# Kernel optimization log

Measured on AMD Instinct MI355X. Metric: run time of the kernel, lower is better.

## Reference

```python
import jax, jax.numpy as jnp
import numpy as np

V, E = 50000, 800000
NODE_IN, EDGE_IN, OUT, HEADS = 128, 16, 32, 4
NEG_SLOPE = 0.2  # DGL EdgeGATConv default negative_slope


def setup_inputs() -> dict:
    key = jax.random.key(0)
    ks = jax.random.split(key, 10)
    return {
        "node_feats": jax.random.normal(ks[0], (V, NODE_IN), jnp.float32),
        "edge_feats": jax.random.normal(ks[1], (E, EDGE_IN), jnp.float32),
        "src": jax.random.randint(ks[2], (E,), 0, V),
        "dst": jax.random.randint(ks[3], (E,), 0, V),
        "W_node": jax.random.normal(ks[4], (NODE_IN, HEADS * OUT), jnp.float32) * 0.05,
        "W_edge": jax.random.normal(ks[5], (EDGE_IN, HEADS * OUT), jnp.float32) * 0.05,
        "attn_l": jax.random.normal(ks[6], (HEADS, OUT), jnp.float32) * 0.05,
        "attn_r": jax.random.normal(ks[7], (HEADS, OUT), jnp.float32) * 0.05,
        "attn_e": jax.random.normal(ks[8], (HEADS, OUT), jnp.float32) * 0.05,
        "res_W": jax.random.normal(ks[9], (NODE_IN, HEADS * OUT), jnp.float32) * 0.05,
        "bias": jnp.zeros((HEADS * OUT,), jnp.float32),
    }


def _leaky_relu(x, slope):
    return jnp.where(x >= 0, x, slope * x)


def reference(node_feats, edge_feats, src, dst, W_node, W_edge, attn_l, attn_r, attn_e, res_W, bias):
    V = node_feats.shape[0]
    H, F = attn_l.shape
    # linear projections
    ft = (node_feats @ W_node).reshape(V, H, F)    # [V,H,F]
    fe = (edge_feats @ W_edge).reshape(-1, H, F)   # [E,H,F]
    # per-head attention logits
    el = jnp.einsum('vhf,hf->vh', ft, attn_l)      # [V,H]
    er = jnp.einsum('vhf,hf->vh', ft, attn_r)      # [V,H]
    ee = jnp.einsum('ehf,hf->eh', fe, attn_e)      # [E,H]
    e = _leaky_relu(el[src] + er[dst] + ee, NEG_SLOPE)  # [E,H]
    # edge softmax over incoming edges of each destination node (stable)
    emax = jax.ops.segment_max(e, dst, num_segments=V)  # [V,H]
    ex = jnp.exp(e - emax[dst])
    esum = jax.ops.segment_sum(ex, dst, num_segments=V)  # [V,H]
    a = ex / esum[dst]                                   # [E,H]
    # weighted message passing: u_mul_e(ft, a) then sum to dst
    msg = ft[src] * a[:, :, None]                        # [E,H,F]
    rst = jax.ops.segment_sum(msg, dst, num_segments=V)  # [V,H,F]
    # residual connection + bias (EdgeGATConv residual=True, bias=True)
    rst = rst + (node_feats @ res_W).reshape(V, H, F)
    rst = rst + bias.reshape(1, H, F)
    # agg_mode='flatten': concat heads
    return rst.reshape(V, H * F)
```

## Files before the change

### kernel.cpp

```cpp
#include <hip/hip_runtime.h>
#include <hip/hip_fp16.h>
#include <cstdint>

#define V_N 50000
#define E_N 800000
#define NODE_IN 128
#define EDGE_IN 16
#define HF 128
#define NEG_SLOPE 0.2f
#define NB_SCAN 196

#define OFF_FT    0
#define OFF_EL    3200000
#define OFF_ER    3400000
#define OFF_DEG   3600000
#define OFF_ROW   3650000
#define OFF_BSUM  3700004
#define OFF_RANK  3700260
#define OFF_REC   4500260
#define OFF_WATT  7700260
#define OFF_BFRAG 7700324

typedef short bf16x8 __attribute__((ext_vector_type(8)));
typedef float f32x4 __attribute__((ext_vector_type(4)));

__device__ __forceinline__ unsigned short f2bf(float f) {
    unsigned u = __float_as_uint(f);
    u += 0x7fffu + ((u >> 16) & 1u);
    return (unsigned short)(u >> 16);
}
__device__ __forceinline__ unsigned pk2(float lo, float hi) {
    return (unsigned)f2bf(lo) | ((unsigned)f2bf(hi) << 16);
}
__device__ __forceinline__ float bflo(unsigned w) { return __uint_as_float(w << 16); }
__device__ __forceinline__ float bfhi(unsigned w) { return __uint_as_float(w & 0xffff0000u); }

typedef __fp16 fp16x2 __attribute__((ext_vector_type(2)));
__device__ __forceinline__ unsigned pkh2(float a, float b) {
    fp16x2 h = __builtin_amdgcn_cvt_pkrtz(a, b);
    return __builtin_bit_cast(unsigned, h);
}
__device__ __forceinline__ __half2 u2h(unsigned u) {
    return __builtin_bit_cast(__half2, u);
}
__device__ __forceinline__ unsigned h2u(__half2 h) {
    return __builtin_bit_cast(unsigned, h);
}

__global__ void k_prep(const float* __restrict__ We,
                       const float* __restrict__ attn_e,
                       const float* __restrict__ Wn,
                       const float* __restrict__ Wr,
                       float* __restrict__ watt,
                       unsigned* __restrict__ bfrag,
                       int* __restrict__ deg) {
    int g = blockIdx.x * 256 + threadIdx.x;
    for (int i = g; i < V_N; i += 16384) deg[i] = 0;
    if (blockIdx.x == 0 && threadIdx.x < 64) {
        int k = threadIdx.x >> 2, h = threadIdx.x & 3;
        float s = 0.f;
        #pragma unroll
        for (int f = 0; f < 32; f++)
            s += We[k * HF + h * 32 + f] * attn_e[h * 32 + f];
        watt[k * 4 + h] = s;
    }
    if (g < 16384) {
        int c    = g >> 8;
        int lane = (g >> 2) & 63;
        int jp   = g & 3;
        int nt = c >> 2, ks = c & 3;
        int col = nt * 16 + (lane & 15);
        int k   = ks * 32 + (lane >> 4) * 8 + jp * 2;
        const float* W = (col < 128) ? Wn : Wr;
        int cc = col & 127;
        float x0 = W[(size_t)k * 128 + cc];
        float x1 = W[(size_t)(k + 1) * 128 + cc];
        bfrag[g] = pk2(x0, x1);
    }
}

__global__ __launch_bounds__(256) void k_node(
    const float* __restrict__ nf, const unsigned* __restrict__ bfragw,
    const float* __restrict__ attn_l, const float* __restrict__ attn_r,
    const float* __restrict__ bias,
    unsigned* __restrict__ ftw, float* __restrict__ el,
    float* __restrict__ er, float* __restrict__ out)
{
    __shared__ __align__(16) float sSf[32 * 140];
    unsigned short* sA = (unsigned short*)sSf;

    const int t = threadIdx.x;
    const int lane = t & 63;
    const int w = t >> 6;
    const int nb = blockIdx.x * 32;
    const int n15 = lane & 15;
    const int q = lane >> 4;
    const unsigned short* bfrag = (const unsigned short*)bfragw;

    #pragma unroll
    for (int i = 0; i < 4; i++) {
        int f = t + i * 256;
        int node = f >> 5;
        int kc = (f & 31) * 4;
        float4 v = {0.f, 0.f, 0.f, 0.f};
        if (nb + node < V_N)
            v = *(const float4*)(nf + (size_t)(nb + node) * NODE_IN + kc);
        uint2 u2 = make_uint2(pk2(v.x, v.y), pk2(v.z, v.w));
        *(uint2*)&sA[node * 136 + kc] = u2;
    }
    __syncthreads();

    f32x4 acc[2][4];
    #pragma unroll
    for (int m = 0; m < 2; m++)
        #pragma unroll
        for (int tt = 0; tt < 4; tt++) acc[m][tt] = (f32x4){0.f, 0.f, 0.f, 0.f};

    #pragma unroll
    for (int ks = 0; ks < 4; ks++) {
        bf16x8 a0 = *(const bf16x8*)&sA[n15 * 136 + ks * 32 + q * 8];
        bf16x8 a1 = *(const bf16x8*)&sA[(16 + n15) * 136 + ks * 32 + q * 8];
        #pragma unroll
        for (int tt = 0; tt < 4; tt++) {
            int nt = (tt < 2) ? (2 * w + tt) : (8 + 2 * w + (tt - 2));
            bf16x8 b = *(const bf16x8*)(bfrag + ((size_t)(nt * 4 + ks) * 64 + lane) * 8);
            acc[0][tt] = __builtin_amdgcn_mfma_f32_16x16x32_bf16(a0, b, acc[0][tt], 0, 0, 0);
            acc[1][tt] = __builtin_amdgcn_mfma_f32_16x16x32_bf16(a1, b, acc[1][tt], 0, 0, 0);
        }
    }

    {
        float al0 = attn_l[w * 32 + n15];
        float al1 = attn_l[w * 32 + 16 + n15];
        float ar0 = attn_r[w * 32 + n15];
        float ar1 = attn_r[w * 32 + 16 + n15];
        #pragma unroll
        for (int m = 0; m < 2; m++) {
            #pragma unroll
            for (int r = 0; r < 4; r++) {
                float fa = acc[m][0][r], fb = acc[m][1][r];
                float elp = fa * al0 + fb * al1;
                float erp = fa * ar0 + fb * ar1;
                elp += __shfl_xor(elp, 1); erp += __shfl_xor(erp, 1);
                elp += __shfl_xor(elp, 2); erp += __shfl_xor(erp, 2);
                elp += __shfl_xor(elp, 4); erp += __shfl_xor(erp, 4);
                elp += __shfl_xor(elp, 8); erp += __shfl_xor(erp, 8);
                int node = nb + m * 16 + q * 4 + r;
                if (n15 == 0 && node < V_N) {
                    el[node * 4 + w] = elp;
                    er[node * 4 + w] = erp;
                }
            }
        }
    }
    #pragma unroll
    for (int m = 0; m < 2; m++)
        #pragma unroll
        for (int r = 0; r < 4; r++) {
            int node = nb + m * 16 + q * 4 + r;
            if (node < V_N)
                ftw[(size_t)node * 64 + w * 16 + n15] =
                    pkh2(acc[m][0][r], acc[m][1][r]);
        }
    __syncthreads();

    #pragma unroll
    for (int m = 0; m < 2; m++)
        #pragma unroll
        for (int tt = 2; tt < 4; tt++)
            #pragma unroll
            for (int r = 0; r < 4; r++)
                sSf[(m * 16 + q * 4 + r) * 140 + w * 32 + (tt - 2) * 16 + n15] =
                    acc[m][tt][r];
    __syncthreads();
    #pragma unroll
    for (int i = 0; i < 4; i++) {
        int u = t + i * 256;
        int node = u >> 5, c4 = (u & 31) * 4;
        if (nb + node < V_N) {
            float4 v = *(float4*)&sSf[node * 140 + c4];
            float4 b4 = *(const float4*)(bias + c4);
            v.x += b4.x; v.y += b4.y; v.z += b4.z; v.w += b4.w;
            *(float4*)(out + (size_t)(nb + node) * HF + c4) = v;
        }
    }
}

__global__ void k_hist(const int* __restrict__ dst, int* __restrict__ deg,
                       int* __restrict__ rank) {
    int e = blockIdx.x * 256 + threadIdx.x;
    if (e < E_N) rank[e] = atomicAdd(&deg[dst[e]], 1);
}

__global__ __launch_bounds__(256) void k_scan1(const int* __restrict__ deg,
                                               int* __restrict__ rowp,
                                               int* __restrict__ bsum) {
    __shared__ int sh[256];
    int t = threadIdx.x, b = blockIdx.x;
    int i = b * 256 + t;
    int v = (i < V_N) ? deg[i] : 0;
    sh[t] = v;
    __syncthreads();
    #pragma unroll
    for (int off = 1; off < 256; off <<= 1) {
        int u = (t >= off) ? sh[t - off] : 0;
        __syncthreads();
        sh[t] += u;
        __syncthreads();
    }
    if (i < V_N) rowp[i] = sh[t] - v;
    if (t == 255) bsum[b] = sh[255];
}

__global__ __launch_bounds__(256) void k_scan23(int* __restrict__ rowp,
                                                const int* __restrict__ bsum) {
    __shared__ int sh[256];
    int t = threadIdx.x, b = blockIdx.x;
    int v = (t < NB_SCAN) ? bsum[t] : 0;
    sh[t] = v;
    __syncthreads();
    #pragma unroll
    for (int off = 1; off < 256; off <<= 1) {
        int u = (t >= off) ? sh[t - off] : 0;
        __syncthreads();
        sh[t] += u;
        __syncthreads();
    }
    int boff = (b == 0) ? 0 : sh[b - 1];
    int i = b * 256 + t;
    if (i < V_N) rowp[i] += boff;
    if (i == 0) rowp[V_N] = E_N;
}

__global__ __launch_bounds__(256) void k_escatter(
    const float* __restrict__ ef, const int* __restrict__ src,
    const int* __restrict__ dst, const int* __restrict__ rank,
    const int* __restrict__ rowp, const float* __restrict__ watt,
    const float* __restrict__ el, uint4* __restrict__ rec)
{
    __shared__ float sw[64];
    __shared__ __align__(16) float see[256][4];
    const int t = threadIdx.x;
    if (t < 64) sw[t] = watt[t];
    __syncthreads();
    const int base = blockIdx.x * 256;
    const int lane = t & 63, w = t >> 6;
    const int k0 = (lane & 3) * 4;

    #pragma unroll
    for (int r = 0; r < 4; r++) {
        int le = w * 64 + r * 16 + (lane >> 2);
        float4 v = *(const float4*)(ef + (size_t)(base + le) * EDGE_IN + k0);
        float e0 = 0.f, e1 = 0.f, e2 = 0.f, e3 = 0.f;
        float vv[4] = {v.x, v.y, v.z, v.w};
        #pragma unroll
        for (int j = 0; j < 4; j++) {
            int k = k0 + j;
            e0 += vv[j] * sw[k * 4 + 0];
            e1 += vv[j] * sw[k * 4 + 1];
            e2 += vv[j] * sw[k * 4 + 2];
            e3 += vv[j] * sw[k * 4 + 3];
        }
        e0 += __shfl_xor(e0, 1); e1 += __shfl_xor(e1, 1);
        e2 += __shfl_xor(e2, 1); e3 += __shfl_xor(e3, 1);
        e0 += __shfl_xor(e0, 2); e1 += __shfl_xor(e1, 2);
        e2 += __shfl_xor(e2, 2); e3 += __shfl_xor(e3, 2);
        if ((lane & 3) == 0) {
            float4 o = {e0, e1, e2, e3};
            *(float4*)&see[le][0] = o;
        }
    }
    __syncthreads();

    int e = base + t;
    int s = src[e], d = dst[e];
    int p = rowp[d] + rank[e];
    float4 ee = *(float4*)&see[t][0];
    float4 el4 = *(const float4*)(el + (size_t)s * 4);
    uint4 rr;
    rr.x = (unsigned)s;
    rr.y = pk2(el4.x + ee.x, el4.y + ee.y);
    rr.z = pk2(el4.z + ee.z, el4.w + ee.w);
    rr.w = 0;
    rec[p] = rr;
}

__global__ __launch_bounds__(256) void k_gather(
    const int* __restrict__ row, const uint4* __restrict__ rec,
    const float* __restrict__ er,
    const unsigned* __restrict__ ftw, float* __restrict__ out)
{
    __shared__ unsigned aw[4][64][4];
    const int lane = threadIdx.x & 63;
    const int wid  = threadIdx.x >> 6;
    const int d = blockIdx.x * 4 + wid;
    if (d >= V_N) return;
    const int n0 = row[d];
    const int deg = row[d + 1] - n0;
    if (deg == 0) return;

    const float4 er4 = *(const float4*)(er + (size_t)d * 4);

    const int qw = lane >> 4, li = lane & 15;
    const int head = li >> 2;
    float4 s4 = {0.f, 0.f, 0.f, 0.f};
    __half2 ha0 = u2h(0u), ha1 = u2h(0u), ha2 = u2h(0u), ha3 = u2h(0u);
    __half2 hb0 = u2h(0u), hb1 = u2h(0u), hb2 = u2h(0u), hb3 = u2h(0u);

    for (int i0 = 0; i0 < deg; i0 += 64) {
        int chunk = min(64, deg - i0);
        int si = 0;
        float4 ex = {0.f, 0.f, 0.f, 0.f};
        if (lane < chunk) {
            uint4 r = rec[n0 + i0 + lane];
            si = (int)r.x;
            float x0 = bflo(r.y) + er4.x;
            float x1 = bfhi(r.y) + er4.y;
            float x2 = bflo(r.z) + er4.z;
            float x3 = bfhi(r.z) + er4.w;
            x0 = x0 >= 0.f ? x0 : NEG_SLOPE * x0;
            x1 = x1 >= 0.f ? x1 : NEG_SLOPE * x1;
            x2 = x2 >= 0.f ? x2 : NEG_SLOPE * x2;
            x3 = x3 >= 0.f ? x3 : NEG_SLOPE * x3;
            ex.x = __expf(x0); ex.y = __expf(x1);
            ex.z = __expf(x2); ex.w = __expf(x3);
            s4.x += ex.x; s4.y += ex.y; s4.z += ex.z; s4.w += ex.w;
        }
        uint4 ap;
        ap.x = pkh2(ex.x, ex.x); ap.y = pkh2(ex.y, ex.y);
        ap.z = pkh2(ex.z, ex.z); ap.w = pkh2(ex.w, ex.w);
        *(uint4*)&aw[wid][lane][0] = ap;
        asm volatile("s_waitcnt lgkmcnt(0)" ::: "memory");

        int iters = (chunk + 7) & ~7;
        for (int j = 0; j < iters; j += 8) {
            int jq0 = j + qw, jq1 = j + qw + 4;
            int sidx0 = __shfl(si, jq0);
            int sidx1 = __shfl(si, jq1);
            unsigned au0 = aw[wid][jq0][head];
            unsigned au1 = aw[wid][jq1][head];
            uint4 wv0 = *(const uint4*)(ftw + (size_t)sidx0 * 64 + li * 4);
            uint4 wv1 = *(const uint4*)(ftw + (size_t)sidx1 * 64 + li * 4);
            ha0 = __hfma2(u2h(wv0.x), u2h(au0), ha0);
            ha1 = __hfma2(u2h(wv0.y), u2h(au0), ha1);
            ha2 = __hfma2(u2h(wv0.z), u2h(au0), ha2);
            ha3 = __hfma2(u2h(wv0.w), u2h(au0), ha3);
            hb0 = __hfma2(u2h(wv1.x), u2h(au1), hb0);
            hb1 = __hfma2(u2h(wv1.y), u2h(au1), hb1);
            hb2 = __hfma2(u2h(wv1.z), u2h(au1), hb2);
            hb3 = __hfma2(u2h(wv1.w), u2h(au1), hb3);
        }
    }
    #pragma unroll
    for (int off = 1; off < 64; off <<= 1) {
        s4.x += __shfl_xor(s4.x, off);
        s4.y += __shfl_xor(s4.y, off);
        s4.z += __shfl_xor(s4.z, off);
        s4.w += __shfl_xor(s4.w, off);
    }
    ha0 = __hadd2(ha0, hb0); ha1 = __hadd2(ha1, hb1);
    ha2 = __hadd2(ha2, hb2); ha3 = __hadd2(ha3, hb3);
    ha0 = __hadd2(ha0, u2h(__shfl_xor(h2u(ha0), 16)));
    ha1 = __hadd2(ha1, u2h(__shfl_xor(h2u(ha1), 16)));
    ha2 = __hadd2(ha2, u2h(__shfl_xor(h2u(ha2), 16)));
    ha3 = __hadd2(ha3, u2h(__shfl_xor(h2u(ha3), 16)));
    ha0 = __hadd2(ha0, u2h(__shfl_xor(h2u(ha0), 32)));
    ha1 = __hadd2(ha1, u2h(__shfl_xor(h2u(ha1), 32)));
    ha2 = __hadd2(ha2, u2h(__shfl_xor(h2u(ha2), 32)));
    ha3 = __hadd2(ha3, u2h(__shfl_xor(h2u(ha3), 32)));
    if (qw == 0) {
        float rsv = 1.f / (head == 0 ? s4.x : head == 1 ? s4.y :
                           head == 2 ? s4.z : s4.w);
        float* op = out + (size_t)d * HF + head * 32 + (li & 3) * 4;
        float4 r0 = *(float4*)op;
        r0.x += __low2float(ha0) * rsv; r0.y += __low2float(ha1) * rsv;
        r0.z += __low2float(ha2) * rsv; r0.w += __low2float(ha3) * rsv;
        *(float4*)op = r0;
        float4 r1 = *(float4*)(op + 16);
        r1.x += __high2float(ha0) * rsv; r1.y += __high2float(ha1) * rsv;
        r1.z += __high2float(ha2) * rsv; r1.w += __high2float(ha3) * rsv;
        *(float4*)(op + 16) = r1;
    }
}

extern "C" void kernel_launch(void* const* d_in, const int* in_sizes, int n_in,
                              void* d_out, int out_size, void* d_ws, size_t ws_size,
                              hipStream_t stream) {
    const float* nf     = (const float*)d_in[0];
    const float* ef     = (const float*)d_in[1];
    const int*   src    = (const int*)d_in[2];
    const int*   dst    = (const int*)d_in[3];
    const float* Wn     = (const float*)d_in[4];
    const float* We     = (const float*)d_in[5];
    const float* attn_l = (const float*)d_in[6];
    const float* attn_r = (const float*)d_in[7];
    const float* attn_e = (const float*)d_in[8];
    const float* Wr     = (const float*)d_in[9];
    const float* bias   = (const float*)d_in[10];
    float* out = (float*)d_out;

    unsigned* wsw  = (unsigned*)d_ws;
    unsigned* ftw  = wsw + OFF_FT;
    float* el      = (float*)(wsw + OFF_EL);
    float* er      = (float*)(wsw + OFF_ER);
    int* deg       = (int*)(wsw + OFF_DEG);
    int* rowp      = (int*)(wsw + OFF_ROW);
    int* bsum      = (int*)(wsw + OFF_BSUM);
    int* rank      = (int*)(wsw + OFF_RANK);
    uint4* rec     = (uint4*)(wsw + OFF_REC);
    float* watt    = (float*)(wsw + OFF_WATT);
    unsigned* bfrag = wsw + OFF_BFRAG;

    k_prep<<<64, 256, 0, stream>>>(We, attn_e, Wn, Wr, watt, bfrag, deg);
    k_hist<<<(E_N + 255) / 256, 256, 0, stream>>>(dst, deg, rank);
    k_scan1<<<NB_SCAN, 256, 0, stream>>>(deg, rowp, bsum);
    k_scan23<<<NB_SCAN, 256, 0, stream>>>(rowp, bsum);
    k_node<<<(V_N + 31) / 32, 256, 0, stream>>>(nf, bfrag, attn_l, attn_r,
                                                bias, ftw, el, er, out);
    k_escatter<<<E_N / 256, 256, 0, stream>>>(ef, src, dst, rank,
                                              rowp, watt, el, rec);
    k_gather<<<(V_N + 3) / 4, 256, 0, stream>>>(rowp, rec, er, ftw, out);
}
```

Before: 245.1 us.

## Fuse histogram, scan and edge scatter into one cooperative persistent kernel

New measurement: 609.3 us. 149% more time.

```diff
diff --git a/kernel.cpp b/kernel.cpp
--- a/kernel.cpp
+++ b/kernel.cpp
@@ -1,6 +1,9 @@
 #include <hip/hip_runtime.h>
 #include <hip/hip_fp16.h>
+#include <hip/hip_cooperative_groups.h>
 #include <cstdint>
+
+namespace cg = cooperative_groups;
 
 #define V_N 50000
 #define E_N 800000
@@ -16,9 +19,7 @@
 #define OFF_DEG   3600000
 #define OFF_ROW   3650000
 #define OFF_BSUM  3700004
-#define OFF_RANK  3700260
 #define OFF_REC   4500260
-#define OFF_WATT  7700260
 #define OFF_BFRAG 7700324
 
 typedef short bf16x8 __attribute__((ext_vector_type(8)));
@@ -47,23 +48,10 @@
     return __builtin_bit_cast(unsigned, h);
 }
 
-__global__ void k_prep(const float* __restrict__ We,
-                       const float* __restrict__ attn_e,
-                       const float* __restrict__ Wn,
+__global__ void k_prep(const float* __restrict__ Wn,
                        const float* __restrict__ Wr,
-                       float* __restrict__ watt,
-                       unsigned* __restrict__ bfrag,
-                       int* __restrict__ deg) {
+                       unsigned* __restrict__ bfrag) {
     int g = blockIdx.x * 256 + threadIdx.x;
-    for (int i = g; i < V_N; i += 16384) deg[i] = 0;
-    if (blockIdx.x == 0 && threadIdx.x < 64) {
-        int k = threadIdx.x >> 2, h = threadIdx.x & 3;
-        float s = 0.f;
-        #pragma unroll
-        for (int f = 0; f < 32; f++)
-            s += We[k * HF + h * 32 + f] * attn_e[h * 32 + f];
-        watt[k * 4 + h] = s;
-    }
     if (g < 16384) {
         int c    = g >> 8;
         int lane = (g >> 2) & 63;
@@ -186,103 +174,124 @@
     }
 }
 
-__global__ void k_hist(const int* __restrict__ dst, int* __restrict__ deg,
-                       int* __restrict__ rank) {
-    int e = blockIdx.x * 256 + threadIdx.x;
-    if (e < E_N) rank[e] = atomicAdd(&deg[dst[e]], 1);
-}
-
-__global__ __launch_bounds__(256) void k_scan1(const int* __restrict__ deg,
-                                               int* __restrict__ rowp,
-                                               int* __restrict__ bsum) {
-    __shared__ int sh[256];
-    int t = threadIdx.x, b = blockIdx.x;
-    int i = b * 256 + t;
-    int v = (i < V_N) ? deg[i] : 0;
-    sh[t] = v;
-    __syncthreads();
-    #pragma unroll
-    for (int off = 1; off < 256; off <<= 1) {
-        int u = (t >= off) ? sh[t - off] : 0;
-        __syncthreads();
-        sh[t] += u;
-        __syncthreads();
-    }
-    if (i < V_N) rowp[i] = sh[t] - v;
-    if (t == 255) bsum[b] = sh[255];
-}
-
-__global__ __launch_bounds__(256) void k_scan23(int* __restrict__ rowp,
-                                                const int* __restrict__ bsum) {
-    __shared__ int sh[256];
-    int t = threadIdx.x, b = blockIdx.x;
-    int v = (t < NB_SCAN) ? bsum[t] : 0;
-    sh[t] = v;
-    __syncthreads();
-    #pragma unroll
-    for (int off = 1; off < 256; off <<= 1) {
-        int u = (t >= off) ? sh[t - off] : 0;
-        __syncthreads();
-        sh[t] += u;
-        __syncthreads();
-    }
-    int boff = (b == 0) ? 0 : sh[b - 1];
-    int i = b * 256 + t;
-    if (i < V_N) rowp[i] += boff;
-    if (i == 0) rowp[V_N] = E_N;
-}
-
-__global__ __launch_bounds__(256) void k_escatter(
+__global__ __launch_bounds__(256, 4) void k_build(
     const float* __restrict__ ef, const int* __restrict__ src,
-    const int* __restrict__ dst, const int* __restrict__ rank,
-    const int* __restrict__ rowp, const float* __restrict__ watt,
-    const float* __restrict__ el, uint4* __restrict__ rec)
+    const int* __restrict__ dst, const float* __restrict__ We,
+    const float* __restrict__ attn_e, const float* __restrict__ el,
+    int* __restrict__ deg, int* __restrict__ rowp,
+    int* __restrict__ bsum, uint4* __restrict__ rec)
 {
+    cg::grid_group grid = cg::this_grid();
     __shared__ float sw[64];
     __shared__ __align__(16) float see[256][4];
+    __shared__ int shs[256];
     const int t = threadIdx.x;
-    if (t < 64) sw[t] = watt[t];
-    __syncthreads();
-    const int base = blockIdx.x * 256;
+    const int b = blockIdx.x;
+    const int G = gridDim.x;
+
+    if (t < 64) {
+        int k = t >> 2, h = t & 3;
+        float s = 0.f;
+        #pragma unroll
+        for (int f = 0; f < 32; f++)
+            s += We[k * HF + h * 32 + f] * attn_e[h * 32 + f];
+        sw[t] = s;
+    }
+    for (int i = b * 256 + t; i < V_N; i += G * 256) deg[i] = 0;
+    grid.sync();
+
     const int lane = t & 63, w = t >> 6;
     const int k0 = (lane & 3) * 4;
-
-    #pragma unroll
-    for (int r = 0; r < 4; r++) {
-        int le = w * 64 + r * 16 + (lane >> 2);
-        float4 v = *(const float4*)(ef + (size_t)(base + le) * EDGE_IN + k0);
-        float e0 = 0.f, e1 = 0.f, e2 = 0.f, e3 = 0.f;
-        float vv[4] = {v.x, v.y, v.z, v.w};
-        #pragma unroll
-        for (int j = 0; j < 4; j++) {
-            int k = k0 + j;
-            e0 += vv[j] * sw[k * 4 + 0];
-            e1 += vv[j] * sw[k * 4 + 1];
-            e2 += vv[j] * sw[k * 4 + 2];
-            e3 += vv[j] * sw[k * 4 + 3];
-        }
-        e0 += __shfl_xor(e0, 1); e1 += __shfl_xor(e1, 1);
-        e2 += __shfl_xor(e2, 1); e3 += __shfl_xor(e3, 1);
-        e0 += __shfl_xor(e0, 2); e1 += __shfl_xor(e1, 2);
-        e2 += __shfl_xor(e2, 2); e3 += __shfl_xor(e3, 2);
-        if ((lane & 3) == 0) {
-            float4 o = {e0, e1, e2, e3};
-            *(float4*)&see[le][0] = o;
-        }
-    }
-    __syncthreads();
-
-    int e = base + t;
-    int s = src[e], d = dst[e];
-    int p = rowp[d] + rank[e];
-    float4 ee = *(float4*)&see[t][0];
-    float4 el4 = *(const float4*)(el + (size_t)s * 4);
-    uint4 rr;
-    rr.x = (unsigned)s;
-    rr.y = pk2(el4.x + ee.x, el4.y + ee.y);
-    rr.z = pk2(el4.z + ee.z, el4.w + ee.w);
-    rr.w = 0;
-    rec[p] = rr;
+    int sv[4], dv[4], rv[4];
+    unsigned lA[4], lB[4];
+    int ntile = 0;
+
+    for (int tile = b; tile < E_N / 256; tile += G) {
+        const int base = tile * 256;
+        #pragma unroll
+        for (int r = 0; r < 4; r++) {
+            int le = w * 64 + r * 16 + (lane >> 2);
+            float4 v = *(const float4*)(ef + (size_t)(base + le) * EDGE_IN + k0);
+            float e0 = 0.f, e1 = 0.f, e2 = 0.f, e3 = 0.f;
+            float vv[4] = {v.x, v.y, v.z, v.w};
+            #pragma unroll
+            for (int j = 0; j < 4; j++) {
+                int k = k0 + j;
+                e0 += vv[j] * sw[k * 4 + 0];
+                e1 += vv[j] * sw[k * 4 + 1];
+                e2 += vv[j] * sw[k * 4 + 2];
+                e3 += vv[j] * sw[k * 4 + 3];
+            }
+            e0 += __shfl_xor(e0, 1); e1 += __shfl_xor(e1, 1);
+            e2 += __shfl_xor(e2, 1); e3 += __shfl_xor(e3, 1);
+            e0 += __shfl_xor(e0, 2); e1 += __shfl_xor(e1, 2);
+            e2 += __shfl_xor(e2, 2); e3 += __shfl_xor(e3, 2);
+            if ((lane & 3) == 0) {
+                float4 o = {e0, e1, e2, e3};
+                *(float4*)&see[le][0] = o;
+            }
+        }
+        __syncthreads();
+        int e = base + t;
+        int s = src[e], d = dst[e];
+        float4 ee = *(float4*)&see[t][0];
+        float4 el4 = *(const float4*)(el + (size_t)s * 4);
+        sv[ntile] = s;
+        dv[ntile] = d;
+        rv[ntile] = atomicAdd(&deg[d], 1);
+        lA[ntile] = pk2(el4.x + ee.x, el4.y + ee.y);
+        lB[ntile] = pk2(el4.z + ee.z, el4.w + ee.w);
+        ntile++;
+        __syncthreads();
+    }
+    grid.sync();
+
+    if (b < NB_SCAN) {
+        int i = b * 256 + t;
+        int v = (i < V_N) ? deg[i] : 0;
+        shs[t] = v;
+        __syncthreads();
+        #pragma unroll
+        for (int off = 1; off < 256; off <<= 1) {
+            int u = (t >= off) ? shs[t - off] : 0;
+            __syncthreads();
+            shs[t] += u;
+            __syncthreads();
+        }
+        if (i < V_N) rowp[i] = shs[t] - v;
+        if (t == 255) bsum[b] = shs[255];
+    }
+    grid.sync();
+    if (b < NB_SCAN) {
+        int v = (t < NB_SCAN) ? bsum[t] : 0;
+        shs[t] = v;
+        __syncthreads();
+        #pragma unroll
+        for (int off = 1; off < 256; off <<= 1) {
+            int u = (t >= off) ? shs[t - off] : 0;
+            __syncthreads();
+            shs[t] += u;
+            __syncthreads();
+        }
+        int boff = (b == 0) ? 0 : shs[b - 1];
+        int i = b * 256 + t;
+        if (i < V_N) rowp[i] += boff;
+        if (i == 0) rowp[V_N] = E_N;
+    }
+    grid.sync();
+
+    #pragma unroll
+    for (int u = 0; u < 4; u++) {
+        if (u < ntile) {
+            int p = rowp[dv[u]] + rv[u];
+            uint4 rr;
+            rr.x = (unsigned)sv[u];
+            rr.y = lA[u];
+            rr.z = lB[u];
+            rr.w = 0;
+            rec[p] = rr;
+        }
+    }
 }
 
 __global__ __launch_bounds__(256) void k_gather(
@@ -406,18 +415,18 @@
     int* deg       = (int*)(wsw + OFF_DEG);
     int* rowp      = (int*)(wsw + OFF_ROW);
     int* bsum      = (int*)(wsw + OFF_BSUM);
-    int* rank      = (int*)(wsw + OFF_RANK);
     uint4* rec     = (uint4*)(wsw + OFF_REC);
-    float* watt    = (float*)(wsw + OFF_WATT);
     unsigned* bfrag = wsw + OFF_BFRAG;
 
-    k_prep<<<64, 256, 0, stream>>>(We, attn_e, Wn, Wr, watt, bfrag, deg);
-    k_hist<<<(E_N + 255) / 256, 256, 0, stream>>>(dst, deg, rank);
-    k_scan1<<<NB_SCAN, 256, 0, stream>>>(deg, rowp, bsum);
-    k_scan23<<<NB_SCAN, 256, 0, stream>>>(rowp, bsum);
+    k_prep<<<64, 256, 0, stream>>>(Wn, Wr, bfrag);
     k_node<<<(V_N + 31) / 32, 256, 0, stream>>>(nf, bfrag, attn_l, attn_r,
                                                 bias, ftw, el, er, out);
-    k_escatter<<<E_N / 256, 256, 0, stream>>>(ef, src, dst, rank,
-                                              rowp, watt, el, rec);
+    {
+        void* args[] = {(void*)&ef, (void*)&src, (void*)&dst, (void*)&We,
+                        (void*)&attn_e, (void*)&el, (void*)&deg, (void*)&rowp,
+                        (void*)&bsum, (void*)&rec};
+        hipLaunchCooperativeKernel((void*)k_build, dim3(1024), dim3(256),
+                                   args, 0, stream);
+    }
     k_gather<<<(V_N + 3) / 4, 256, 0, stream>>>(rowp, rec, er, ftw, out);
 }
```

## Fuse two-pass scan into single-pass decoupled look-back scan

Applied to the files above, without the earlier changes.

After: 255.1 us. 4.1% more time.

```diff
diff --git a/kernel.cpp b/kernel.cpp
--- a/kernel.cpp
+++ b/kernel.cpp
@@ -15,11 +15,10 @@
 #define OFF_ER    3400000
 #define OFF_DEG   3600000
 #define OFF_ROW   3650000
-#define OFF_BSUM  3700004
-#define OFF_RANK  3700260
-#define OFF_REC   4500260
-#define OFF_WATT  7700260
-#define OFF_BFRAG 7700324
+#define OFF_ST    3700004
+#define OFF_RANK  3700400
+#define OFF_REC   4500400
+#define OFF_BFRAG 7700400
 
 typedef short bf16x8 __attribute__((ext_vector_type(8)));
 typedef float f32x4 __attribute__((ext_vector_type(4)));
@@ -47,23 +46,14 @@
     return __builtin_bit_cast(unsigned, h);
 }
 
-__global__ void k_prep(const float* __restrict__ We,
-                       const float* __restrict__ attn_e,
-                       const float* __restrict__ Wn,
+__global__ void k_prep(const float* __restrict__ Wn,
                        const float* __restrict__ Wr,
-                       float* __restrict__ watt,
                        unsigned* __restrict__ bfrag,
-                       int* __restrict__ deg) {
+                       int* __restrict__ deg,
+                       unsigned long long* __restrict__ st) {
     int g = blockIdx.x * 256 + threadIdx.x;
     for (int i = g; i < V_N; i += 16384) deg[i] = 0;
-    if (blockIdx.x == 0 && threadIdx.x < 64) {
-        int k = threadIdx.x >> 2, h = threadIdx.x & 3;
-        float s = 0.f;
-        #pragma unroll
-        for (int f = 0; f < 32; f++)
-            s += We[k * HF + h * 32 + f] * attn_e[h * 32 + f];
-        watt[k * 4 + h] = s;
-    }
+    if (g < NB_SCAN) st[g] = 0ULL;
     if (g < 16384) {
         int c    = g >> 8;
         int lane = (g >> 2) & 63;
@@ -188,14 +178,20 @@
 
 __global__ void k_hist(const int* __restrict__ dst, int* __restrict__ deg,
                        int* __restrict__ rank) {
-    int e = blockIdx.x * 256 + threadIdx.x;
-    if (e < E_N) rank[e] = atomicAdd(&deg[dst[e]], 1);
-}
-
-__global__ __launch_bounds__(256) void k_scan1(const int* __restrict__ deg,
-                                               int* __restrict__ rowp,
-                                               int* __restrict__ bsum) {
+    int base = blockIdx.x * 1024 + threadIdx.x;
+    #pragma unroll
+    for (int u = 0; u < 4; u++) {
+        int e = base + u * 256;
+        if (e < E_N) rank[e] = atomicAdd(&deg[dst[e]], 1);
+    }
+}
+
+__global__ __launch_bounds__(256) void k_scan(
+    const int* __restrict__ deg, int* __restrict__ rowp,
+    unsigned long long* __restrict__ st)
+{
     __shared__ int sh[256];
+    __shared__ int sexcl;
     int t = threadIdx.x, b = blockIdx.x;
     int i = b * 256 + t;
     int v = (i < V_N) ? deg[i] : 0;
@@ -208,40 +204,50 @@
         sh[t] += u;
         __syncthreads();
     }
-    if (i < V_N) rowp[i] = sh[t] - v;
-    if (t == 255) bsum[b] = sh[255];
-}
-
-__global__ __launch_bounds__(256) void k_scan23(int* __restrict__ rowp,
-                                                const int* __restrict__ bsum) {
-    __shared__ int sh[256];
-    int t = threadIdx.x, b = blockIdx.x;
-    int v = (t < NB_SCAN) ? bsum[t] : 0;
-    sh[t] = v;
-    __syncthreads();
-    #pragma unroll
-    for (int off = 1; off < 256; off <<= 1) {
-        int u = (t >= off) ? sh[t - off] : 0;
-        __syncthreads();
-        sh[t] += u;
-        __syncthreads();
-    }
-    int boff = (b == 0) ? 0 : sh[b - 1];
-    int i = b * 256 + t;
-    if (i < V_N) rowp[i] += boff;
-    if (i == 0) rowp[V_N] = E_N;
+    int agg = sh[255];
+    if (t == 0) {
+        if (b == 0) {
+            atomicExch(&st[0], (2ULL << 32) | (unsigned)agg);
+            sexcl = 0;
+        } else {
+            atomicExch(&st[b], (1ULL << 32) | (unsigned)agg);
+            int excl = 0;
+            int j = b - 1;
+            while (true) {
+                unsigned long long p = atomicAdd(&st[j], 0ULL);
+                unsigned stat = (unsigned)(p >> 32);
+                if (stat == 2u) { excl += (int)(unsigned)p; break; }
+                if (stat == 1u) { excl += (int)(unsigned)p; j--; continue; }
+                __builtin_amdgcn_s_sleep(1);
+            }
+            atomicExch(&st[b], (2ULL << 32) | (unsigned)(excl + agg));
+            sexcl = excl;
+        }
+    }
+    __syncthreads();
+    int excl = sexcl;
+    if (i < V_N) rowp[i] = excl + sh[t] - v;
+    if (b == 0 && t == 0) rowp[V_N] = E_N;
 }
 
 __global__ __launch_bounds__(256) void k_escatter(
     const float* __restrict__ ef, const int* __restrict__ src,
     const int* __restrict__ dst, const int* __restrict__ rank,
-    const int* __restrict__ rowp, const float* __restrict__ watt,
+    const int* __restrict__ rowp, const float* __restrict__ We,
+    const float* __restrict__ attn_e,
     const float* __restrict__ el, uint4* __restrict__ rec)
 {
     __shared__ float sw[64];
     __shared__ __align__(16) float see[256][4];
     const int t = threadIdx.x;
-    if (t < 64) sw[t] = watt[t];
+    if (t < 64) {
+        int k = t >> 2, h = t & 3;
+        float s = 0.f;
+        #pragma unroll
+        for (int f = 0; f < 32; f++)
+            s += We[k * HF + h * 32 + f] * attn_e[h * 32 + f];
+        sw[t] = s;
+    }
     __syncthreads();
     const int base = blockIdx.x * 256;
     const int lane = t & 63, w = t >> 6;
@@ -405,19 +411,17 @@
     float* er      = (float*)(wsw + OFF_ER);
     int* deg       = (int*)(wsw + OFF_DEG);
     int* rowp      = (int*)(wsw + OFF_ROW);
-    int* bsum      = (int*)(wsw + OFF_BSUM);
+    unsigned long long* st = (unsigned long long*)(wsw + OFF_ST);
     int* rank      = (int*)(wsw + OFF_RANK);
     uint4* rec     = (uint4*)(wsw + OFF_REC);
-    float* watt    = (float*)(wsw + OFF_WATT);
     unsigned* bfrag = wsw + OFF_BFRAG;
 
-    k_prep<<<64, 256, 0, stream>>>(We, attn_e, Wn, Wr, watt, bfrag, deg);
-    k_hist<<<(E_N + 255) / 256, 256, 0, stream>>>(dst, deg, rank);
-    k_scan1<<<NB_SCAN, 256, 0, stream>>>(deg, rowp, bsum);
-    k_scan23<<<NB_SCAN, 256, 0, stream>>>(rowp, bsum);
+    k_prep<<<64, 256, 0, stream>>>(Wn, Wr, bfrag, deg, st);
+    k_hist<<<(E_N + 1023) / 1024, 256, 0, stream>>>(dst, deg, rank);
+    k_scan<<<NB_SCAN, 256, 0, stream>>>(deg, rowp, st);
     k_node<<<(V_N + 31) / 32, 256, 0, stream>>>(nf, bfrag, attn_l, attn_r,
                                                 bias, ftw, el, er, out);
-    k_escatter<<<E_N / 256, 256, 0, stream>>>(ef, src, dst, rank,
-                                              rowp, watt, el, rec);
+    k_escatter<<<E_N / 256, 256, 0, stream>>>(ef, src, dst, rank, rowp,
+                                              We, attn_e, el, rec);
     k_gather<<<(V_N + 3) / 4, 256, 0, stream>>>(rowp, rec, er, ftw, out);
 }
```
